# Kernel tuning notes

Hardware: AMD Instinct MI355X
Metric: run time of the kernel (lower is better)

The kernel has to match this reference:

```python
import jax, jax.numpy as jnp
import numpy as np

B, N, S, K, D = 8, 8192, 1024, 32, 64
RADIUS = 0.2
MLP = [64, 64, 128]
C_IN = 3 + D


def _fps(pts):
    # pts: [N,3] -> [S] farthest-point indices (deterministic start at index 0,
    # matching pytorch3d.sample_farthest_points default random_start_point=False)
    def body(carry, _):
        d, last = carry
        dd = jnp.sum((pts - pts[last]) ** 2, axis=-1)
        d = jnp.minimum(d, dd)
        return (d, jnp.argmax(d)), last
    init = (jnp.full((pts.shape[0],), 1e10, pts.dtype), jnp.asarray(0))
    _, idxs = jax.lax.scan(body, init, None, length=S)
    return idxs


def _ball_query(new_xyz, xyz):
    # new_xyz [B,S,3], xyz [B,N,3] -> idx [B,S,K]
    # classic PointNet++ ball query: first K points (by index order) within radius;
    # queries with fewer than K neighbors are padded by replicating the first hit.
    sqr = jnp.sum((new_xyz[:, :, None, :] - xyz[:, None, :, :]) ** 2, axis=-1)  # [B,S,N]
    cand = jnp.where(sqr <= RADIUS ** 2,
                     jnp.arange(N, dtype=jnp.int32)[None, None, :],
                     jnp.int32(N))
    idx = -jax.lax.top_k(-cand, K)[0]  # K smallest valid indices, ascending
    first = idx[..., :1]
    return jnp.where(idx == N, first, idx)


def _gather(arr, idx):
    # arr [B,N,C], idx [B,S,K] -> [B,S,K,C]
    return jax.vmap(lambda a, i: a[i])(arr, idx)


def _forward(xyz, points, attention, w0, b0, w1, b1, w2, b2):
    x = xyz.transpose(0, 2, 1)        # [B,N,3]
    p = points.transpose(0, 2, 1)     # [B,N,D]
    a = attention.transpose(0, 2, 1)  # [B,N,1]
    fps_idx = jax.vmap(_fps)(x)                      # [B,S]
    new_xyz = jax.vmap(lambda q, i: q[i])(x, fps_idx)  # [B,S,3]
    idx = _ball_query(new_xyz, x)                    # [B,S,K]
    g_norm = _gather(x, idx) - new_xyz[:, :, None, :]   # [B,S,K,3]
    feat = jnp.concatenate([g_norm, _gather(p, idx)], axis=-1)  # [B,S,K,3+D]
    new_att = jnp.mean(_gather(a, idx), axis=-2).reshape(x.shape[0], 1, -1)  # [B,1,S]
    # shared MLP (1x1 Conv2d == per-point dense), no BN (bn=False)
    h = jax.nn.relu(jnp.einsum('bskc,oc->bsko', feat, w0) + b0)
    h = jax.nn.relu(jnp.einsum('bskc,oc->bsko', h, w1) + b1)
    h = jax.nn.relu(jnp.einsum('bskc,oc->bsko', h, w2) + b2)
    new_points = jnp.max(h, axis=2)  # max-pool over nsample -> [B,S,C_out]
    return new_xyz.transpose(0, 2, 1), new_points.transpose(0, 2, 1), new_att


def setup_inputs() -> dict:
    key = jax.random.key(0)
    ks = jax.random.split(key, 9)
    xyz = jax.random.uniform(ks[0], (B, 3, N), dtype=jnp.float32)  # unit cube
    points = jax.random.normal(ks[1], (B, D, N), dtype=jnp.float32)
    attention = jax.random.uniform(ks[2], (B, 1, N), dtype=jnp.float32)
    cin = C_IN
    w0 = jax.random.normal(ks[3], (MLP[0], cin), dtype=jnp.float32) / np.sqrt(cin)
    b0 = jnp.zeros((MLP[0],), jnp.float32)
    w1 = jax.random.normal(ks[4], (MLP[1], MLP[0]), dtype=jnp.float32) / np.sqrt(MLP[0])
    b1 = jnp.zeros((MLP[1],), jnp.float32)
    w2 = jax.random.normal(ks[5], (MLP[2], MLP[1]), dtype=jnp.float32) / np.sqrt(MLP[1])
    b2 = jnp.zeros((MLP[2],), jnp.float32)
    return {"xyz": xyz, "points": points, "attention": attention,
            "w0": w0, "b0": b0, "w1": w1, "b1": b1, "w2": w2, "b2": b2}


def reference(xyz, points, attention, w0, b0, w1, b1, w2, b2):
    return _forward(xyz, points, attention, w0, b0, w1, b1, w2, b2)
```

## Files before the change

kernel.cpp:

```cpp
#include <hip/hip_runtime.h>

#define NPTS 8192
#define NSAMP 1024
#define NBATCH 8
#define KNB 32

typedef float f32x2 __attribute__((ext_vector_type(2)));
typedef unsigned long long u64;

__device__ __forceinline__ f32x2 pk_add(f32x2 a, f32x2 b) {
  f32x2 d; asm("v_pk_add_f32 %0, %1, %2" : "=v"(d) : "v"(a), "v"(b)); return d;
}
__device__ __forceinline__ f32x2 pk_mul(f32x2 a, f32x2 b) {
  f32x2 d; asm("v_pk_mul_f32 %0, %1, %2" : "=v"(d) : "v"(a), "v"(b)); return d;
}

#define DPP_FMAX_ROUND(v, CTRL)                                                        \
  do {                                                                                 \
    int _b = __float_as_int(v);                                                        \
    int _p = __builtin_amdgcn_update_dpp(_b, _b, CTRL, 0xF, 0xF, false);               \
    (v) = fmaxf((v), __int_as_float(_p));                                              \
  } while (0)

#define DPP_FMIN_ROUND(v, CTRL)                                                        \
  do {                                                                                 \
    int _b = __float_as_int(v);                                                        \
    int _p = __builtin_amdgcn_update_dpp(_b, _b, CTRL, 0xF, 0xF, false);               \
    (v) = fminf((v), __int_as_float(_p));                                              \
  } while (0)

#define DPP_MIN_ROUND(k, CTRL)                                                         \
  do {                                                                                 \
    unsigned _lo = (unsigned)(k), _hi = (unsigned)((k) >> 32);                         \
    unsigned _plo = (unsigned)__builtin_amdgcn_update_dpp((int)_lo, (int)_lo, CTRL,    \
                                                          0xF, 0xF, false);            \
    unsigned _phi = (unsigned)__builtin_amdgcn_update_dpp((int)_hi, (int)_hi, CTRL,    \
                                                          0xF, 0xF, false);            \
    u64 _ok = (((u64)_phi) << 32) | _plo;                                              \
    if (_ok < (k)) (k) = _ok;                                                          \
  } while (0)

__device__ __forceinline__ float sqdist_rn(float px, float py, float pz,
                                           float qx, float qy, float qz) {
  float dx = px - qx, dy = py - qy, dz = pz - qz;
  return __fadd_rn(__fadd_rn(__fmul_rn(dx, dx), __fmul_rn(dy, dy)), __fmul_rn(dz, dz));
}

__global__ __launch_bounds__(512) void fps_kernel(const float* __restrict__ xyz,
                                                  float* __restrict__ out_newxyz) {
  __shared__ __align__(16) char smem_raw[NPTS * 3 * 4];
  u64* sbuf = reinterpret_cast<u64*>(smem_raw);
  float* cds = reinterpret_cast<float*>(smem_raw);
  __shared__ u64 wkeys[2][8];

  const int b = blockIdx.x;
  const int tid = threadIdx.x;
  const int lane = tid & 63;
  const int wv = tid >> 6;
  const float* xb = xyz + (size_t)b * 3 * NPTS;

  for (int j = 0; j < 16; j++) {
    int n = tid + j * 512;
    float x = xb[n];
    sbuf[n] = (((u64)__float_as_uint(x)) << 32) | (u64)n;
  }
  __syncthreads();

  for (unsigned k = 2; k <= (unsigned)NPTS; k <<= 1) {
    for (unsigned jm = k >> 1; jm > 0; jm >>= 1) {
      for (int p = 0; p < 16; p++) {
        unsigned i = (unsigned)tid + (unsigned)p * 512u;
        unsigned ixj = i ^ jm;
        if (ixj > i) {
          u64 a = sbuf[i], c = sbuf[ixj];
          bool up = ((i & k) == 0);
          if ((a > c) == up) { sbuf[i] = c; sbuf[ixj] = a; }
        }
      }
      __syncthreads();
    }
  }

  f32x2 X2[8], Y2[8], Z2[8], D2[8];
  unsigned idxp[8];
  float txmin = 1e30f, txmax = -1e30f;
#pragma unroll
  for (int j = 0; j < 8; j++) {
    u64 k0 = sbuf[tid * 16 + 2 * j];
    u64 k1 = sbuf[tid * 16 + 2 * j + 1];
    unsigned n0 = (unsigned)k0 & 8191u, n1 = (unsigned)k1 & 8191u;
    float x0 = __uint_as_float((unsigned)(k0 >> 32));
    float x1 = __uint_as_float((unsigned)(k1 >> 32));
    X2[j].x = x0; X2[j].y = x1;
    Y2[j].x = xb[NPTS + n0];     Y2[j].y = xb[NPTS + n1];
    Z2[j].x = xb[2 * NPTS + n0]; Z2[j].y = xb[2 * NPTS + n1];
    D2[j].x = 1e10f;             D2[j].y = 1e10f;
    idxp[j] = n0 | (n1 << 16);
    txmin = fminf(txmin, fminf(x0, x1));
    txmax = fmaxf(txmax, fmaxf(x0, x1));
  }
  DPP_FMIN_ROUND(txmin, 0x111); DPP_FMIN_ROUND(txmin, 0x112);
  DPP_FMIN_ROUND(txmin, 0x114); DPP_FMIN_ROUND(txmin, 0x118);
  DPP_FMIN_ROUND(txmin, 0x142); DPP_FMIN_ROUND(txmin, 0x143);
  DPP_FMAX_ROUND(txmax, 0x111); DPP_FMAX_ROUND(txmax, 0x112);
  DPP_FMAX_ROUND(txmax, 0x114); DPP_FMAX_ROUND(txmax, 0x118);
  DPP_FMAX_ROUND(txmax, 0x142); DPP_FMAX_ROUND(txmax, 0x143);
  const float xlo = __int_as_float(__builtin_amdgcn_readlane(__float_as_int(txmin), 63));
  const float xhi = __int_as_float(__builtin_amdgcn_readlane(__float_as_int(txmax), 63));
  __syncthreads();

#pragma unroll
  for (int j = 0; j < 8; j++) {
    unsigned n0 = idxp[j] & 0xFFFFu, n1 = idxp[j] >> 16;
    cds[n0 * 3 + 0] = X2[j].x; cds[n0 * 3 + 1] = Y2[j].x; cds[n0 * 3 + 2] = Z2[j].x;
    cds[n1 * 3 + 0] = X2[j].y; cds[n1 * 3 + 1] = Y2[j].y; cds[n1 * 3 + 2] = Z2[j].y;
  }
  __syncthreads();

  float sx = cds[0], sy = cds[1], sz = cds[2];
  unsigned c0i = 0, c1i = 0;
  float bv_cache = 1e10f;
  u64 key_cache = ~0ull;

  for (int t = 0; t < NSAMP; t++) {
    float gap = fmaxf(fmaxf(xlo - sx, sx - xhi), 0.0f);
    float lb = __fmul_rn(gap, gap);

    if (lb < bv_cache) {
      f32x2 nqx, nqy, nqz;
      nqx.x = -sx; nqx.y = -sx;
      nqy.x = -sy; nqy.y = -sy;
      nqz.x = -sz; nqz.y = -sz;
      float bvx = -1.0f, bvy = -1.0f;
#pragma unroll
      for (int j = 0; j < 8; j++) {
        f32x2 dx = pk_add(X2[j], nqx);
        f32x2 dy = pk_add(Y2[j], nqy);
        f32x2 dz = pk_add(Z2[j], nqz);
        f32x2 dd = pk_add(pk_add(pk_mul(dx, dx), pk_mul(dy, dy)), pk_mul(dz, dz));
        float m0 = fminf(D2[j].x, dd.x);
        float m1 = fminf(D2[j].y, dd.y);
        D2[j].x = m0;
        D2[j].y = m1;
        bvx = fmaxf(bvx, m0);
        bvy = fmaxf(bvy, m1);
      }
      const float bvl = fmaxf(bvx, bvy);

      float bvr = bvl;
      DPP_FMAX_ROUND(bvr, 0x111);
      DPP_FMAX_ROUND(bvr, 0x112);
      DPP_FMAX_ROUND(bvr, 0x114);
      DPP_FMAX_ROUND(bvr, 0x118);
      DPP_FMAX_ROUND(bvr, 0x142);
      DPP_FMAX_ROUND(bvr, 0x143);

      unsigned cand = 0xFFFFFFFFu;
#pragma unroll
      for (int j = 0; j < 8; j++) {
        unsigned n0 = idxp[j] & 0xFFFFu, n1 = idxp[j] >> 16;
        if (D2[j].y == bvl && n1 < cand) cand = n1;
        if (D2[j].x == bvl && n0 < cand) cand = n0;
      }

      float wval = __int_as_float(__builtin_amdgcn_readlane(__float_as_int(bvr), 63));

      unsigned long long mask = __ballot(bvl == wval);
      unsigned cm = 0xFFFFFFFFu;
      while (mask) {
        int l = __builtin_ctzll(mask);
        unsigned c = (unsigned)__builtin_amdgcn_readlane((int)cand, l);
        cm = c < cm ? c : cm;
        mask &= mask - 1;
      }

      key_cache = (((u64)(~__float_as_uint(wval))) << 32) | (u64)cm;
      bv_cache = wval;
    }

    const int par = t & 1;
    if (lane == 0) wkeys[par][wv] = key_cache;
    __syncthreads();
    u64 k8 = wkeys[par][lane & 7];
    DPP_MIN_ROUND(k8, 0xB1);
    DPP_MIN_ROUND(k8, 0x4E);
    DPP_MIN_ROUND(k8, 0x141);
    unsigned wid = (unsigned)__builtin_amdgcn_readfirstlane((int)(unsigned)k8);

    if (t + 1 == tid) c0i = wid;
    if (t + 1 == tid + 512) c1i = wid;

    sx = cds[wid * 3 + 0];
    sy = cds[wid * 3 + 1];
    sz = cds[wid * 3 + 2];
  }

  {
    float ax = cds[c0i * 3 + 0], ay = cds[c0i * 3 + 1], az = cds[c0i * 3 + 2];
    float bx = cds[c1i * 3 + 0], by = cds[c1i * 3 + 1], bz = cds[c1i * 3 + 2];
    out_newxyz[(b * 3 + 0) * NSAMP + tid] = ax;
    out_newxyz[(b * 3 + 1) * NSAMP + tid] = ay;
    out_newxyz[(b * 3 + 2) * NSAMP + tid] = az;
    out_newxyz[(b * 3 + 0) * NSAMP + 512 + tid] = bx;
    out_newxyz[(b * 3 + 1) * NSAMP + 512 + tid] = by;
    out_newxyz[(b * 3 + 2) * NSAMP + 512 + tid] = bz;
  }
}

__global__ __launch_bounds__(256) void ballq_kernel(const float* __restrict__ xyz,
                                                    const float* __restrict__ att,
                                                    const float* __restrict__ newxyz,
                                                    int* __restrict__ idx_out,
                                                    float* __restrict__ att_out) {
  __shared__ int rowbuf[4][KNB];
  const int wv = threadIdx.x >> 6;
  const int lane = threadIdx.x & 63;
  const int g = blockIdx.x * 4 + wv;
  const int b = g >> 10;
  const int s = g & 1023;
  const float* xb = xyz + (size_t)b * 3 * NPTS;

  float qx = newxyz[(b * 3 + 0) * NSAMP + s];
  float qy = newxyz[(b * 3 + 1) * NSAMP + s];
  float qz = newxyz[(b * 3 + 2) * NSAMP + s];

  int have = 0;
  int firstn = 0;
  for (int c = 0; c < NPTS / 64; c++) {
    int n = c * 64 + lane;
    float dd = sqdist_rn(xb[n], xb[NPTS + n], xb[2 * NPTS + n], qx, qy, qz);
    bool inb = (dd <= 0.04f);
    unsigned long long m = __ballot(inb);
    if (have == 0 && m != 0ull) firstn = c * 64 + __builtin_ctzll(m);
    int pre = __popcll(m & ((1ull << lane) - 1ull));
    if (inb && (have + pre) < KNB) rowbuf[wv][have + pre] = n;
    have += __popcll(m);
    if (have >= KNB) break;
  }
  if (have > KNB) have = KNB;
  if (lane < KNB && lane >= have) rowbuf[wv][lane] = firstn;

  float av = 0.0f;
  if (lane < KNB) {
    int myidx = rowbuf[wv][lane];
    idx_out[(size_t)g * KNB + lane] = myidx;
    av = att[(size_t)b * NPTS + myidx];
  }
#pragma unroll
  for (int m = 1; m < 64; m <<= 1) av += __shfl_xor(av, m, 64);
  if (lane == 0) att_out[g] = av * 0.03125f;
}

__global__ __launch_bounds__(256) void mlp_kernel(
    const float* __restrict__ xyz, const float* __restrict__ pts,
    const float* __restrict__ newxyz, const int* __restrict__ idx,
    const float* __restrict__ w0, const float* __restrict__ b0,
    const float* __restrict__ w1, const float* __restrict__ b1,
    const float* __restrict__ w2, const float* __restrict__ b2,
    float* __restrict__ out_np) {
  const int g = blockIdx.x;
  const int b = g >> 10;
  const int s = g & 1023;
  const int t = threadIdx.x;

  __shared__ __align__(16) float feat[67 * 32];
  __shared__ __align__(16) float h0s[64 * 36];
  __shared__ __align__(16) float h1s[64 * 36];
  __shared__ int sidx[KNB];

  if (t < KNB) sidx[t] = idx[(size_t)g * KNB + t];
  __syncthreads();

  {
    int k = t & 31, rg = t >> 5;
    int n = sidx[k];
    const float* pb = pts + (size_t)b * 64 * NPTS;
    for (int r = rg; r < 67; r += 8) {
      float v;
      if (r < 3)
        v = xyz[((size_t)b * 3 + r) * NPTS + n] - newxyz[(b * 3 + r) * NSAMP + s];
      else
        v = pb[(size_t)(r - 3) * NPTS + n];
      feat[r * 32 + k] = v;
    }
  }
  __syncthreads();

  const int kq = t & 7;
  const int og = t >> 3;

  {
    float a0[8];
    float bu = b0[2 * og], bw = b0[2 * og + 1];
    a0[0] = a0[1] = a0[2] = a0[3] = bu;
    a0[4] = a0[5] = a0[6] = a0[7] = bw;
    const float* wr0 = w0 + (2 * og) * 67;
    const float* wr1 = wr0 + 67;
    for (int c = 0; c < 67; c++) {
      float4 f = *(const float4*)&feat[c * 32 + kq * 4];
      float u = wr0[c], v = wr1[c];
      a0[0] = fmaf(u, f.x, a0[0]); a0[1] = fmaf(u, f.y, a0[1]);
      a0[2] = fmaf(u, f.z, a0[2]); a0[3] = fmaf(u, f.w, a0[3]);
      a0[4] = fmaf(v, f.x, a0[4]); a0[5] = fmaf(v, f.y, a0[5]);
      a0[6] = fmaf(v, f.z, a0[6]); a0[7] = fmaf(v, f.w, a0[7]);
    }
    float4 r0, r1;
    r0.x = fmaxf(a0[0], 0.f); r0.y = fmaxf(a0[1], 0.f);
    r0.z = fmaxf(a0[2], 0.f); r0.w = fmaxf(a0[3], 0.f);
    r1.x = fmaxf(a0[4], 0.f); r1.y = fmaxf(a0[5], 0.f);
    r1.z = fmaxf(a0[6], 0.f); r1.w = fmaxf(a0[7], 0.f);
    *(float4*)&h0s[(2 * og) * 36 + kq * 4] = r0;
    *(float4*)&h0s[(2 * og + 1) * 36 + kq * 4] = r1;
  }
  __syncthreads();

  {
    float a1[8];
    float bu = b1[2 * og], bw = b1[2 * og + 1];
    a1[0] = a1[1] = a1[2] = a1[3] = bu;
    a1[4] = a1[5] = a1[6] = a1[7] = bw;
    const float* wr0 = w1 + (2 * og) * 64;
    const float* wr1 = wr0 + 64;
    for (int c = 0; c < 64; c++) {
      float4 f = *(const float4*)&h0s[c * 36 + kq * 4];
      float u = wr0[c], v = wr1[c];
      a1[0] = fmaf(u, f.x, a1[0]); a1[1] = fmaf(u, f.y, a1[1]);
      a1[2] = fmaf(u, f.z, a1[2]); a1[3] = fmaf(u, f.w, a1[3]);
      a1[4] = fmaf(v, f.x, a1[4]); a1[5] = fmaf(v, f.y, a1[5]);
      a1[6] = fmaf(v, f.z, a1[6]); a1[7] = fmaf(v, f.w, a1[7]);
    }
    float4 r0, r1;
    r0.x = fmaxf(a1[0], 0.f); r0.y = fmaxf(a1[1], 0.f);
    r0.z = fmaxf(a1[2], 0.f); r0.w = fmaxf(a1[3], 0.f);
    r1.x = fmaxf(a1[4], 0.f); r1.y = fmaxf(a1[5], 0.f);
    r1.z = fmaxf(a1[6], 0.f); r1.w = fmaxf(a1[7], 0.f);
    *(float4*)&h1s[(2 * og) * 36 + kq * 4] = r0;
    *(float4*)&h1s[(2 * og + 1) * 36 + kq * 4] = r1;
  }
  __syncthreads();

  {
    const int kq2 = t & 3;
    const int og2 = t >> 2;
    float a2[16];
    float bu = b2[2 * og2], bw = b2[2 * og2 + 1];
#pragma unroll
    for (int i = 0; i < 8; i++) { a2[i] = bu; a2[8 + i] = bw; }
    const float* wr0 = w2 + (2 * og2) * 64;
    const float* wr1 = wr0 + 64;
    for (int c = 0; c < 64; c++) {
      float4 fA = *(const float4*)&h1s[c * 36 + kq2 * 8];
      float4 fB = *(const float4*)&h1s[c * 36 + kq2 * 8 + 4];
      float u = wr0[c], v = wr1[c];
      a2[0] = fmaf(u, fA.x, a2[0]);  a2[1] = fmaf(u, fA.y, a2[1]);
      a2[2] = fmaf(u, fA.z, a2[2]);  a2[3] = fmaf(u, fA.w, a2[3]);
      a2[4] = fmaf(u, fB.x, a2[4]);  a2[5] = fmaf(u, fB.y, a2[5]);
      a2[6] = fmaf(u, fB.z, a2[6]);  a2[7] = fmaf(u, fB.w, a2[7]);
      a2[8] = fmaf(v, fA.x, a2[8]);  a2[9] = fmaf(v, fA.y, a2[9]);
      a2[10] = fmaf(v, fA.z, a2[10]); a2[11] = fmaf(v, fA.w, a2[11]);
      a2[12] = fmaf(v, fB.x, a2[12]); a2[13] = fmaf(v, fB.y, a2[13]);
      a2[14] = fmaf(v, fB.z, a2[14]); a2[15] = fmaf(v, fB.w, a2[15]);
    }
    float m0 = a2[0], m1 = a2[8];
#pragma unroll
    for (int i = 1; i < 8; i++) { m0 = fmaxf(m0, a2[i]); m1 = fmaxf(m1, a2[8 + i]); }
    m0 = fmaxf(m0, 0.f);
    m1 = fmaxf(m1, 0.f);
    m0 = fmaxf(m0, __shfl_xor(m0, 1, 64));
    m0 = fmaxf(m0, __shfl_xor(m0, 2, 64));
    m1 = fmaxf(m1, __shfl_xor(m1, 1, 64));
    m1 = fmaxf(m1, __shfl_xor(m1, 2, 64));
    if (kq2 == 0) {
      out_np[((size_t)b * 128 + 2 * og2) * NSAMP + s] = m0;
      out_np[((size_t)b * 128 + 2 * og2 + 1) * NSAMP + s] = m1;
    }
  }
}

extern "C" void kernel_launch(void* const* d_in, const int* in_sizes, int n_in,
                              void* d_out, int out_size, void* d_ws, size_t ws_size,
                              hipStream_t stream) {
  (void)in_sizes; (void)n_in; (void)out_size; (void)ws_size;
  const float* xyz = (const float*)d_in[0];
  const float* pts = (const float*)d_in[1];
  const float* att = (const float*)d_in[2];
  const float* w0 = (const float*)d_in[3];
  const float* b0 = (const float*)d_in[4];
  const float* w1 = (const float*)d_in[5];
  const float* b1 = (const float*)d_in[6];
  const float* w2 = (const float*)d_in[7];
  const float* b2 = (const float*)d_in[8];

  float* out = (float*)d_out;
  float* out_newxyz = out;
  float* out_newpts = out + NBATCH * 3 * NSAMP;
  float* out_att = out + NBATCH * 3 * NSAMP + NBATCH * 128 * NSAMP;
  int* idx_ws = (int*)d_ws;

  fps_kernel<<<NBATCH, 512, 0, stream>>>(xyz, out_newxyz);
  ballq_kernel<<<(NBATCH * NSAMP) / 4, 256, 0, stream>>>(xyz, att, out_newxyz, idx_ws, out_att);
  mlp_kernel<<<NBATCH * NSAMP, 256, 0, stream>>>(xyz, pts, out_newxyz, idx_ws,
                                                 w0, b0, w1, b1, w2, b2, out_newpts);
}
```

Before: 1.173 ms.

## Replace per-wave FPS argmax reduction with per-thread keys reduced block-wide

```diff
diff --git a/kernel.cpp b/kernel.cpp
--- a/kernel.cpp
+++ b/kernel.cpp
@@ -40,6 +40,8 @@
     if (_ok < (k)) (k) = _ok;                                                          \
   } while (0)
 
+__device__ __forceinline__ u64 umin64(u64 a, u64 b) { return a < b ? a : b; }
+
 __device__ __forceinline__ float sqdist_rn(float px, float py, float pz,
                                            float qx, float qy, float qz) {
   float dx = px - qx, dy = py - qy, dz = pz - qz;
@@ -51,12 +53,11 @@
   __shared__ __align__(16) char smem_raw[NPTS * 3 * 4];
   u64* sbuf = reinterpret_cast<u64*>(smem_raw);
   float* cds = reinterpret_cast<float*>(smem_raw);
-  __shared__ u64 wkeys[2][8];
+  __shared__ u64 wkeys[2][512];
 
   const int b = blockIdx.x;
   const int tid = threadIdx.x;
   const int lane = tid & 63;
-  const int wv = tid >> 6;
   const float* xb = xyz + (size_t)b * 3 * NPTS;
 
   for (int j = 0; j < 16; j++) {
@@ -119,14 +120,15 @@
 
   float sx = cds[0], sy = cds[1], sz = cds[2];
   unsigned c0i = 0, c1i = 0;
-  float bv_cache = 1e10f;
+  float gmax = 1e30f;
   u64 key_cache = ~0ull;
 
   for (int t = 0; t < NSAMP; t++) {
     float gap = fmaxf(fmaxf(xlo - sx, sx - xhi), 0.0f);
     float lb = __fmul_rn(gap, gap);
-
-    if (lb < bv_cache) {
+    const int par = t & 1;
+
+    if (lb < gmax) {
       f32x2 nqx, nqy, nqz;
       nqx.x = -sx; nqx.y = -sx;
       nqy.x = -sy; nqy.y = -sy;
@@ -147,14 +149,6 @@
       }
       const float bvl = fmaxf(bvx, bvy);
 
-      float bvr = bvl;
-      DPP_FMAX_ROUND(bvr, 0x111);
-      DPP_FMAX_ROUND(bvr, 0x112);
-      DPP_FMAX_ROUND(bvr, 0x114);
-      DPP_FMAX_ROUND(bvr, 0x118);
-      DPP_FMAX_ROUND(bvr, 0x142);
-      DPP_FMAX_ROUND(bvr, 0x143);
-
       unsigned cand = 0xFFFFFFFFu;
 #pragma unroll
       for (int j = 0; j < 8; j++) {
@@ -163,29 +157,32 @@
         if (D2[j].x == bvl && n0 < cand) cand = n0;
       }
 
-      float wval = __int_as_float(__builtin_amdgcn_readlane(__float_as_int(bvr), 63));
-
-      unsigned long long mask = __ballot(bvl == wval);
-      unsigned cm = 0xFFFFFFFFu;
-      while (mask) {
-        int l = __builtin_ctzll(mask);
-        unsigned c = (unsigned)__builtin_amdgcn_readlane((int)cand, l);
-        cm = c < cm ? c : cm;
-        mask &= mask - 1;
-      }
-
-      key_cache = (((u64)(~__float_as_uint(wval))) << 32) | (u64)cm;
-      bv_cache = wval;
-    }
-
-    const int par = t & 1;
-    if (lane == 0) wkeys[par][wv] = key_cache;
+      key_cache = (((u64)(~__float_as_uint(bvl))) << 32) | (u64)cand;
+    }
+    wkeys[par][tid] = key_cache;
     __syncthreads();
-    u64 k8 = wkeys[par][lane & 7];
-    DPP_MIN_ROUND(k8, 0xB1);
-    DPP_MIN_ROUND(k8, 0x4E);
-    DPP_MIN_ROUND(k8, 0x141);
-    unsigned wid = (unsigned)__builtin_amdgcn_readfirstlane((int)(unsigned)k8);
+
+    u64 k0 = wkeys[par][lane];
+    u64 k1 = wkeys[par][64 + lane];
+    u64 k2 = wkeys[par][128 + lane];
+    u64 k3 = wkeys[par][192 + lane];
+    u64 k4 = wkeys[par][256 + lane];
+    u64 k5 = wkeys[par][320 + lane];
+    u64 k6 = wkeys[par][384 + lane];
+    u64 k7 = wkeys[par][448 + lane];
+    u64 ka = umin64(umin64(k0, k1), umin64(k2, k3));
+    u64 kb = umin64(umin64(k4, k5), umin64(k6, k7));
+    u64 k = umin64(ka, kb);
+    DPP_MIN_ROUND(k, 0x111);
+    DPP_MIN_ROUND(k, 0x112);
+    DPP_MIN_ROUND(k, 0x114);
+    DPP_MIN_ROUND(k, 0x118);
+    DPP_MIN_ROUND(k, 0x142);
+    DPP_MIN_ROUND(k, 0x143);
+    unsigned wlo = (unsigned)__builtin_amdgcn_readlane((int)(unsigned)k, 63);
+    unsigned whi = (unsigned)__builtin_amdgcn_readlane((int)(unsigned)(k >> 32), 63);
+    unsigned wid = wlo & 8191u;
+    gmax = __uint_as_float(~whi);
 
     if (t + 1 == tid) c0i = wid;
     if (t + 1 == tid + 512) c1i = wid;
```

After: 1.339 ms. 14.2% more time.
